# Kernel tuning notes

Measured on AMD Instinct MI355X. Metric: run time of the kernel, lower is better.

The kernel has to match this reference:

```python
import jax, jax.numpy as jnp
import numpy as np

N = 8192        # nodes
IN_DIM = 512
OUT_DIM = 512
NUM_HEADS = 1   # required for view(-1,3)/view(-1,1,1) consistency in original code
K_NEIGH = 16


def setup_inputs() -> dict:
    key = jax.random.key(0)
    k0, k1, k2, k3, k4 = jax.random.split(key, 5)
    s = 1.0 / np.sqrt(IN_DIM)
    h = jax.random.normal(k0, (N, IN_DIM), dtype=jnp.float32)
    # nn.Linear default init: U(-1/sqrt(fan_in), 1/sqrt(fan_in)), bias=False
    Wq = jax.random.uniform(k1, (OUT_DIM * NUM_HEADS, IN_DIM), jnp.float32, -s, s)
    Wk = jax.random.uniform(k2, (OUT_DIM * NUM_HEADS, IN_DIM), jnp.float32, -s, s)
    Wv = jax.random.uniform(k3, (OUT_DIM * NUM_HEADS, IN_DIM), jnp.float32, -s, s)
    Wg = jax.random.uniform(k4, (3 * NUM_HEADS, IN_DIM), jnp.float32, -s, s)
    return {"h": h, "Wq": Wq, "Wk": Wk, "Wv": Wv, "Wg": Wg}


def _knn_edges(coords, k):
    # dgl.knn_graph semantics: each node receives edges from its k nearest
    # points (self included). src = neighbor, dst = query node.
    sq = jnp.sum(coords * coords, axis=-1)                      # [N]
    neg_d2 = 2.0 * (coords @ coords.T) - sq[:, None] - sq[None, :]  # -||xi-xj||^2, [N,N]
    _, idx = jax.lax.top_k(neg_d2, k)                           # [N,k] nearest per row
    n = coords.shape[0]
    src = idx.reshape(-1)                                       # [N*k]
    dst = jnp.repeat(jnp.arange(n, dtype=idx.dtype), k)         # [N*k]
    return src, dst


def reference(h, Wq, Wk, Wv, Wg):
    n = h.shape[0]
    D = OUT_DIM
    scale = jnp.float32(np.sqrt(D))

    Q_h = (h @ Wq.T).reshape(n, NUM_HEADS, D)
    K_h = (h @ Wk.T).reshape(n, NUM_HEADS, D)
    V_h = (h @ Wv.T).reshape(n, NUM_HEADS, D)
    G_h = (h @ Wg.T).reshape(n, NUM_HEADS, 3)

    coords = G_h.reshape(n, 3)  # num_heads == 1
    src, dst = _knn_edges(coords, K_NEIGH)  # E = n * K_NEIGH edges

    # edge-wise attention score: exp(clip((K_src . Q_dst)/sqrt(D), -5, 5))
    score = jnp.sum(K_h[src] * Q_h[dst], axis=-1, keepdims=True)     # [E,1,1]
    score_e = jnp.exp(jnp.clip(score / scale, -5.0, 5.0))

    # distance decay: exp(clip(-||G_src - G_dst|| / sqrt(D), -5, 5))
    dist = -jnp.sqrt(jnp.sum((G_h[src] - G_h[dst]) ** 2, axis=-1) + 1e-6)  # [E,1]
    distance = jnp.exp(jnp.clip(dist / scale, -5.0, 5.0))

    weight = score_e.reshape(-1, 1, 1) * distance.reshape(-1, 1, 1)  # [E,1,1]
    v1 = weight * V_h[src]                                           # [E,1,D]

    wV = jax.ops.segment_sum(v1, dst, num_segments=n)                # [n,1,D]
    z = jax.ops.segment_sum(score_e, dst, num_segments=n)            # [n,1,1]
    z = jnp.broadcast_to(z.reshape(n, 1, 1), (n, 1, D))

    mask = z > 0
    out = jnp.where(mask, wV / jnp.where(mask, z, 1.0), wV)
    return out
```

## Files before the change

kernel.cpp:

```cpp
#include <hip/hip_runtime.h>
#include <hip/hip_bf16.h>
#include <math.h>

#define N_NODES 8192
#define IN_DIM  512
#define OUT_DIM 512
#define KN      16
#define CAP     128
#define QPB     8

typedef __attribute__((ext_vector_type(8))) short bf16x8;
typedef __attribute__((ext_vector_type(4))) float f32x4;

__device__ __forceinline__ ushort f2bf(float x) {
  __hip_bfloat16 b = __float2bfloat16(x);
  return *reinterpret_cast<ushort*>(&b);
}
__device__ __forceinline__ float bflo(unsigned u) { return __uint_as_float(u << 16); }
__device__ __forceinline__ float bfhi(unsigned u) { return __uint_as_float(u & 0xffff0000u); }

#define GLOAD_LDS16(gp, lp)                                                     \
  __builtin_amdgcn_global_load_lds((const __attribute__((address_space(1))) void*)(gp), \
                                   (__attribute__((address_space(3))) void*)(lp), 16, 0, 0)

__global__ __launch_bounds__(256) void prep_kernel(
    const float* __restrict__ h, const float* __restrict__ Wg,
    ushort* __restrict__ A2,
    double* __restrict__ Gx, double* __restrict__ Gy,
    double* __restrict__ Gz, double* __restrict__ Gsq,
    float4* __restrict__ gpk) {
  const int node = (blockIdx.x * 256 + threadIdx.x) >> 6;
  const int lane = threadIdx.x & 63;
  const int k = lane * 8;
  const float* hr = h + (size_t)node * IN_DIM;

  float4 v0 = *(const float4*)&hr[k];
  float4 v1 = *(const float4*)&hr[k + 4];

  ushort h0 = f2bf(v0.x), h1 = f2bf(v0.y), h2 = f2bf(v0.z), h3 = f2bf(v0.w);
  ushort h4 = f2bf(v1.x), h5 = f2bf(v1.y), h6 = f2bf(v1.z), h7 = f2bf(v1.w);
  ushort4 hiA = make_ushort4(h0, h1, h2, h3);
  ushort4 hiB = make_ushort4(h4, h5, h6, h7);
  ushort4 loA = make_ushort4(f2bf(v0.x - bflo((unsigned)h0)), f2bf(v0.y - bflo((unsigned)h1)),
                             f2bf(v0.z - bflo((unsigned)h2)), f2bf(v0.w - bflo((unsigned)h3)));
  ushort4 loB = make_ushort4(f2bf(v1.x - bflo((unsigned)h4)), f2bf(v1.y - bflo((unsigned)h5)),
                             f2bf(v1.z - bflo((unsigned)h6)), f2bf(v1.w - bflo((unsigned)h7)));
  size_t base = (size_t)node * 1024 + k;
  *(ushort4*)&A2[base]           = hiA;
  *(ushort4*)&A2[base + 4]       = hiB;
  *(ushort4*)&A2[base + 512]     = loA;
  *(ushort4*)&A2[base + 512 + 4] = loB;

  float4 w0a = *(const float4*)&Wg[0 * IN_DIM + k];
  float4 w0b = *(const float4*)&Wg[0 * IN_DIM + k + 4];
  float4 w1a = *(const float4*)&Wg[1 * IN_DIM + k];
  float4 w1b = *(const float4*)&Wg[1 * IN_DIM + k + 4];
  float4 w2a = *(const float4*)&Wg[2 * IN_DIM + k];
  float4 w2b = *(const float4*)&Wg[2 * IN_DIM + k + 4];

  double s0 = 0.0, s1 = 0.0, s2 = 0.0;
  s0 += (double)v0.x * w0a.x; s0 += (double)v0.y * w0a.y;
  s0 += (double)v0.z * w0a.z; s0 += (double)v0.w * w0a.w;
  s0 += (double)v1.x * w0b.x; s0 += (double)v1.y * w0b.y;
  s0 += (double)v1.z * w0b.z; s0 += (double)v1.w * w0b.w;
  s1 += (double)v0.x * w1a.x; s1 += (double)v0.y * w1a.y;
  s1 += (double)v0.z * w1a.z; s1 += (double)v0.w * w1a.w;
  s1 += (double)v1.x * w1b.x; s1 += (double)v1.y * w1b.y;
  s1 += (double)v1.z * w1b.z; s1 += (double)v1.w * w1b.w;
  s2 += (double)v0.x * w2a.x; s2 += (double)v0.y * w2a.y;
  s2 += (double)v0.z * w2a.z; s2 += (double)v0.w * w2a.w;
  s2 += (double)v1.x * w2b.x; s2 += (double)v1.y * w2b.y;
  s2 += (double)v1.z * w2b.z; s2 += (double)v1.w * w2b.w;

  #pragma unroll
  for (int off = 32; off; off >>= 1) {
    s0 += __shfl_down(s0, off);
    s1 += __shfl_down(s1, off);
    s2 += __shfl_down(s2, off);
  }
  if (lane == 0) {
    double sq = s0 * s0 + s1 * s1 + s2 * s2;
    Gx[node] = s0; Gy[node] = s1; Gz[node] = s2; Gsq[node] = sq;
    gpk[node] = make_float4((float)s0, (float)s1, (float)s2, -(float)sq);
  }
}

__global__ __launch_bounds__(256) void split_w(const float* __restrict__ Wq,
                                               const float* __restrict__ Wk,
                                               const float* __restrict__ Wv,
                                               ushort* __restrict__ Bqk,
                                               ushort* __restrict__ Bv) {
  int i = blockIdx.x * 256 + threadIdx.x;
  int n  = i >> 7;
  int kc = (i & 127) << 2;
  if (n < 1024) {
    const float* W = (n < 512) ? Wq : Wk;
    int r = n & 511;
    float4 v = *(const float4*)&W[(size_t)r * 512 + kc];
    *(ushort4*)&Bqk[(size_t)n * 512 + kc] =
        make_ushort4(f2bf(v.x), f2bf(v.y), f2bf(v.z), f2bf(v.w));
  } else {
    int r = n - 1024;
    float4 v = *(const float4*)&Wv[(size_t)r * 512 + kc];
    ushort4 hv = make_ushort4(f2bf(v.x), f2bf(v.y), f2bf(v.z), f2bf(v.w));
    *(ushort4*)&Bv[(size_t)r * 1024 + kc]       = hv;
    *(ushort4*)&Bv[(size_t)r * 1024 + 512 + kc] = hv;
  }
}

#define GEMM_BLOCKS 768
#define SM_BYTES 20544

__global__ __launch_bounds__(256) void gemm_knn(
    const ushort* __restrict__ A2, const ushort* __restrict__ Bqk,
    const ushort* __restrict__ Bv,
    ushort* __restrict__ Q2, ushort* __restrict__ K2, ushort* __restrict__ V2,
    const float4* __restrict__ gpk,
    const double* __restrict__ Gx, const double* __restrict__ Gy,
    const double* __restrict__ Gz, const double* __restrict__ Gsq,
    int* __restrict__ knn) {
  __shared__ unsigned long long smraw[SM_BYTES / 8];
  const int tid = threadIdx.x, w = tid >> 6, lane = tid & 63;

  if (blockIdx.x < GEMM_BLOCKS) {
    const int id = blockIdx.x;
    const int sw = (id & 7) * 96 + (id >> 3);
    const int bm = sw / 12, bn = sw % 12;
    const int wr = w >> 1, wc = w & 1;
    const bool isv = (bn >= 8);
    const int  kmax = isv ? 1024 : 512;
    const int  ldb  = isv ? 1024 : 512;
    const ushort* Bb = isv ? (Bv + (size_t)(bn - 8) * 128 * 1024)
                           : (Bqk + (size_t)bn * 128 * 512);
    ushort* lA = (ushort*)smraw;
    ushort* lB = lA + 128 * 32;

    f32x4 acc[4][4] = {};

    const int   srow = w * 32 + (lane >> 2);
    const int   scol = (lane & 3) * 8;
    const size_t gA0 = (size_t)(bm * 128 + srow) * 1024 + scol;
    const size_t gB0 = (size_t)srow * ldb + scol;

    for (int k0 = 0; k0 < kmax; k0 += 32) {
      GLOAD_LDS16(&A2[gA0 + k0],                  &lA[w * 1024]);
      GLOAD_LDS16(&A2[gA0 + 16 * 1024 + k0],      &lA[w * 1024 + 512]);
      GLOAD_LDS16(&Bb[gB0 + k0],                  &lB[w * 1024]);
      GLOAD_LDS16(&Bb[gB0 + (size_t)16 * ldb + k0], &lB[w * 1024 + 512]);
      __syncthreads();

      const int ar = wr * 64 + (lane & 15);
      const int br = wc * 64 + (lane & 15);
      const int kc = (lane >> 4) * 8;
      bf16x8 af[4], bfr[4];
      #pragma unroll
      for (int f = 0; f < 4; ++f) {
        af[f]  = *(const bf16x8*)&lA[(ar + f * 16) * 32 + kc];
        bfr[f] = *(const bf16x8*)&lB[(br + f * 16) * 32 + kc];
      }
      #pragma unroll
      for (int fm = 0; fm < 4; ++fm)
        #pragma unroll
        for (int fn = 0; fn < 4; ++fn)
          acc[fm][fn] = __builtin_amdgcn_mfma_f32_16x16x32_bf16(af[fm], bfr[fn], acc[fm][fn], 0, 0, 0);
      __syncthreads();
    }

    ushort* Cm = isv ? V2 : (bn < 4 ? Q2 : K2);
    const int col  = (isv ? (bn - 8) : (bn & 3)) * 128 + wc * 64 + (lane & 15);
    const int row0 = bm * 128 + wr * 64 + (lane >> 4) * 4;
    #pragma unroll
    for (int fm = 0; fm < 4; ++fm)
      #pragma unroll
      for (int fn = 0; fn < 4; ++fn)
        #pragma unroll
        for (int r = 0; r < 4; ++r)
          Cm[(size_t)(row0 + fm * 16 + r) * 512 + col + fn * 16] = f2bf(acc[fm][fn][r]);
  } else {
    const int qbase = (blockIdx.x - GEMM_BLOCKS) * QPB;
    float (*s_tmax)[256] = (float(*)[256])smraw;
    int   (*s_cand)[CAP] = (int(*)[CAP])((char*)smraw + 8192);
    double(*s_dval)[CAP] = (double(*)[CAP])((char*)smraw + 12288);
    int*   s_cnt = (int*)((char*)smraw + 20480);
    float* s_T   = (float*)((char*)smraw + 20512);

    float q2x[QPB], q2y[QPB], q2z[QPB], tmax[QPB];
    #pragma unroll
    for (int s = 0; s < QPB; ++s) {
      float4 qv = gpk[qbase + s];
      q2x[s] = 2.f * qv.x; q2y[s] = 2.f * qv.y; q2z[s] = 2.f * qv.z;
      tmax[s] = -1e30f;
    }
    if (tid < QPB) s_cnt[tid] = 0;

    {
      float4 c0 = gpk[tid];
      float4 c1 = gpk[tid + 256];
      for (int i = 0; i < 16; ++i) {
        int nx = ((i + 1) & 15) * 512;
        float4 n0 = gpk[tid + nx];
        float4 n1 = gpk[tid + nx + 256];
        #pragma unroll
        for (int s = 0; s < QPB; ++s) {
          float v0 = fmaf(q2x[s], c0.x, fmaf(q2y[s], c0.y, fmaf(q2z[s], c0.z, c0.w)));
          float v1 = fmaf(q2x[s], c1.x, fmaf(q2y[s], c1.y, fmaf(q2z[s], c1.z, c1.w)));
          tmax[s] = fmaxf(fmaxf(tmax[s], v0), v1);
        }
        c0 = n0; c1 = n1;
      }
    }
    #pragma unroll
    for (int s = 0; s < QPB; ++s) s_tmax[s][tid] = tmax[s];
    __syncthreads();

    #pragma unroll
    for (int qq = 0; qq < 2; ++qq) {
      int q = w * 2 + qq;
      float v = fmaxf(fmaxf(s_tmax[q][lane], s_tmax[q][lane + 64]),
                      fmaxf(s_tmax[q][lane + 128], s_tmax[q][lane + 192]));
      unsigned b = __float_as_uint(v);
      unsigned u = b ^ ((unsigned)((int)b >> 31) | 0x80000000u);
      unsigned thr = 0;
      for (int bit = 31; bit >= 0; --bit) {
        unsigned cand = thr | (1u << bit);
        unsigned long long m = __ballot(u >= cand);
        if (__popcll(m) >= KN) thr = cand;
      }
      unsigned tb = (thr & 0x80000000u) ? (thr ^ 0x80000000u) : ~thr;
      if (lane == 0) s_T[q] = __uint_as_float(tb);
    }
    __syncthreads();

    float Ts[QPB];
    #pragma unroll
    for (int s = 0; s < QPB; ++s) Ts[s] = s_T[s];
    {
      float4 c0 = gpk[tid];
      float4 c1 = gpk[tid + 256];
      for (int i = 0; i < 16; ++i) {
        int nx = ((i + 1) & 15) * 512;
        float4 n0 = gpk[tid + nx];
        float4 n1 = gpk[tid + nx + 256];
        int j0 = tid + i * 512, j1 = j0 + 256;
        #pragma unroll
        for (int s = 0; s < QPB; ++s) {
          float v0 = fmaf(q2x[s], c0.x, fmaf(q2y[s], c0.y, fmaf(q2z[s], c0.z, c0.w)));
          float v1 = fmaf(q2x[s], c1.x, fmaf(q2y[s], c1.y, fmaf(q2z[s], c1.z, c1.w)));
          if (v0 >= Ts[s]) { int p = atomicAdd(&s_cnt[s], 1); if (p < CAP) s_cand[s][p] = j0; }
          if (v1 >= Ts[s]) { int p = atomicAdd(&s_cnt[s], 1); if (p < CAP) s_cand[s][p] = j1; }
        }
        c0 = n0; c1 = n1;
      }
    }
    __syncthreads();

    const int qA = w * 2, qB = qA + 1;
    const int cntA = min(s_cnt[qA], CAP);
    const int cntB = min(s_cnt[qB], CAP);
    int j0a = -1, j1a = -1, j0b = -1, j1b = -1;
    double v0a = 0, v1a = 0, v0b = 0, v1b = 0;
    {
      int gq = qbase + qA;
      double xi = Gx[gq], yi = Gy[gq], zi = Gz[gq], sqi = Gsq[gq];
      if (lane < cntA) {
        j0a = s_cand[qA][lane];
        v0a = 2.0 * (xi * Gx[j0a] + yi * Gy[j0a] + zi * Gz[j0a]) - sqi - Gsq[j0a];
        s_dval[qA][lane] = v0a;
      }
      if (lane + 64 < cntA) {
        j1a = s_cand[qA][lane + 64];
        v1a = 2.0 * (xi * Gx[j1a] + yi * Gy[j1a] + zi * Gz[j1a]) - sqi - Gsq[j1a];
        s_dval[qA][lane + 64] = v1a;
      }
    }
    {
      int gq = qbase + qB;
      double xi = Gx[gq], yi = Gy[gq], zi = Gz[gq], sqi = Gsq[gq];
      if (lane < cntB) {
        j0b = s_cand[qB][lane];
        v0b = 2.0 * (xi * Gx[j0b] + yi * Gy[j0b] + zi * Gz[j0b]) - sqi - Gsq[j0b];
        s_dval[qB][lane] = v0b;
      }
      if (lane + 64 < cntB) {
        j1b = s_cand[qB][lane + 64];
        v1b = 2.0 * (xi * Gx[j1b] + yi * Gy[j1b] + zi * Gz[j1b]) - sqi - Gsq[j1b];
        s_dval[qB][lane + 64] = v1b;
      }
    }
    __syncthreads();
    {
      int r0 = 0, r1 = 0;
      for (int m = 0; m < cntA; ++m) {
        double dv = s_dval[qA][m]; int di = s_cand[qA][m];
        r0 += (dv > v0a) || (dv == v0a && di < j0a);
        r1 += (dv > v1a) || (dv == v1a && di < j1a);
      }
      int gq = qbase + qA;
      if (j0a >= 0 && r0 < KN) knn[gq * KN + r0] = j0a;
      if (j1a >= 0 && r1 < KN) knn[gq * KN + r1] = j1a;
    }
    {
      int r0 = 0, r1 = 0;
      for (int m = 0; m < cntB; ++m) {
        double dv = s_dval[qB][m]; int di = s_cand[qB][m];
        r0 += (dv > v0b) || (dv == v0b && di < j0b);
        r1 += (dv > v1b) || (dv == v1b && di < j1b);
      }
      int gq = qbase + qB;
      if (j0b >= 0 && r0 < KN) knn[gq * KN + r0] = j0b;
      if (j1b >= 0 && r1 < KN) knn[gq * KN + r1] = j1b;
    }
  }
}

__global__ __launch_bounds__(256) void attend_kernel(
    const ushort* __restrict__ Q2, const ushort* __restrict__ K2, const ushort* __restrict__ V2,
    const float4* __restrict__ gpk,
    const int* __restrict__ knn, float* __restrict__ out) {
  const int i    = blockIdx.x;
  const int tid  = threadIdx.x;
  const int wv   = tid >> 6;
  const int lane = tid & 63;

  __shared__ int   s_idx[KN];
  __shared__ float s_w[KN];
  __shared__ float s_se[KN];

  if (tid < KN) s_idx[tid] = knn[i * KN + tid];
  __syncthreads();

  uint4 qa = *(const uint4*)&Q2[(size_t)i * 512 + lane * 8];
  float q0 = bflo(qa.x), q1 = bfhi(qa.x), q2 = bflo(qa.y), q3 = bfhi(qa.y);
  float q4 = bflo(qa.z), q5 = bfhi(qa.z), q6 = bflo(qa.w), q7 = bfhi(qa.w);

  float partial[4];
  #pragma unroll
  for (int s = 0; s < 4; ++s) {
    int src = s_idx[wv * 4 + s];
    uint4 ka = *(const uint4*)&K2[(size_t)src * 512 + lane * 8];
    float acc = q0 * bflo(ka.x);
    acc = fmaf(q1, bfhi(ka.x), acc);
    acc = fmaf(q2, bflo(ka.y), acc);
    acc = fmaf(q3, bfhi(ka.y), acc);
    acc = fmaf(q4, bflo(ka.z), acc);
    acc = fmaf(q5, bfhi(ka.z), acc);
    acc = fmaf(q6, bflo(ka.w), acc);
    acc = fmaf(q7, bfhi(ka.w), acc);
    partial[s] = acc;
  }
  #pragma unroll
  for (int s = 0; s < 4; ++s)
    #pragma unroll
    for (int off = 32; off; off >>= 1) partial[s] += __shfl_down(partial[s], off);

  if (lane == 0) {
    float4 gi = gpk[i];
    #pragma unroll
    for (int s = 0; s < 4; ++s) {
      int e = wv * 4 + s;
      int src = s_idx[e];
      float sc = partial[s] / 22.627417f;
      sc = fminf(fmaxf(sc, -5.f), 5.f);
      float se = expf(sc);
      float4 gs = gpk[src];
      float dx = gi.x - gs.x, dy = gi.y - gs.y, dz = gi.z - gs.z;
      float dd = -sqrtf(fmaf(dx, dx, fmaf(dy, dy, fmaf(dz, dz, 1e-6f))));
      float dc = fminf(fmaxf(dd / 22.627417f, -5.f), 5.f);
      float de = expf(dc);
      s_se[e] = se;
      s_w[e]  = se * de;
    }
  }
  __syncthreads();

  float z = 0.f;
  #pragma unroll
  for (int e = 0; e < KN; ++e) z += s_se[e];

  const int d = tid * 2;
  float a0 = 0.f, a1 = 0.f;
  #pragma unroll
  for (int e = 0; e < KN; ++e) {
    unsigned vv = *(const unsigned*)&V2[(size_t)s_idx[e] * 512 + d];
    a0 = fmaf(s_w[e], bflo(vv), a0);
    a1 = fmaf(s_w[e], bfhi(vv), a1);
  }
  float inv = (z > 0.f) ? (1.f / z) : 1.f;
  float2 o = make_float2(a0 * inv, a1 * inv);
  *(float2*)&out[(size_t)i * 512 + d] = o;
}

extern "C" void kernel_launch(void* const* d_in, const int* in_sizes, int n_in,
                              void* d_out, int out_size, void* d_ws, size_t ws_size,
                              hipStream_t stream) {
  const float* h  = (const float*)d_in[0];
  const float* Wq = (const float*)d_in[1];
  const float* Wk = (const float*)d_in[2];
  const float* Wv = (const float*)d_in[3];
  const float* Wg = (const float*)d_in[4];
  float* out = (float*)d_out;

  char* ws = (char*)d_ws;
  ushort* A2  = (ushort*)(ws);
  ushort* Bqk = (ushort*)(ws + (16u << 20));
  ushort* Bv  = (ushort*)(ws + (17u << 20));
  ushort* Q2  = (ushort*)(ws + (18u << 20));
  ushort* K2  = (ushort*)(ws + (26u << 20));
  ushort* V2  = (ushort*)(ws + (34u << 20));
  float4* gpk = (float4*)(ws + (42u << 20));
  double* Gx  = (double*)(ws + (42u << 20) + (1u << 17));
  double* Gy  = Gx + N_NODES;
  double* Gz  = Gy + N_NODES;
  double* Gsq = Gz + N_NODES;
  int*    knn = (int*)(Gsq + N_NODES);

  hipLaunchKernelGGL(prep_kernel, dim3(N_NODES / 4), dim3(256), 0, stream,
                     h, Wg, A2, Gx, Gy, Gz, Gsq, gpk);
  hipLaunchKernelGGL(split_w, dim3(768), dim3(256), 0, stream,
                     Wq, Wk, Wv, Bqk, Bv);
  hipLaunchKernelGGL(gemm_knn, dim3(GEMM_BLOCKS + N_NODES / QPB), dim3(256), 0, stream,
                     A2, Bqk, Bv, Q2, K2, V2, gpk, Gx, Gy, Gz, Gsq, knn);
  hipLaunchKernelGGL(attend_kernel, dim3(N_NODES), dim3(256), 0, stream,
                     Q2, K2, V2, gpk, knn, out);
}
```

Measured before the change: 113.7 us.

## Merge prep and weight-split kernels; separate fused GEMM/KNN into two launches

The h-prep and weight-conversion kernels become one launch with block-index dispatch, which removes one launch and lets the two independent prep jobs run concurrently. The previously fused GEMM+KNN kernel is split into a dedicated QKV GEMM kernel and a separate KNN kernel, each with its own statically sized shared memory. The split gives up the overlap of GEMM and KNN blocks inside one launch and serializes the two phases. In exchange each kernel gets its own resource footprint and occupancy, with no block-index branch.

```diff
diff --git a/kernel.cpp b/kernel.cpp
--- a/kernel.cpp
+++ b/kernel.cpp
@@ -23,293 +23,290 @@
   __builtin_amdgcn_global_load_lds((const __attribute__((address_space(1))) void*)(gp), \
                                    (__attribute__((address_space(3))) void*)(lp), 16, 0, 0)
 
-__global__ __launch_bounds__(256) void prep_kernel(
+__global__ __launch_bounds__(256) void prep_split(
     const float* __restrict__ h, const float* __restrict__ Wg,
-    ushort* __restrict__ A2,
+    const float* __restrict__ Wq, const float* __restrict__ Wk,
+    const float* __restrict__ Wv,
+    ushort* __restrict__ A2, ushort* __restrict__ Bqk, ushort* __restrict__ Bv,
     double* __restrict__ Gx, double* __restrict__ Gy,
     double* __restrict__ Gz, double* __restrict__ Gsq,
     float4* __restrict__ gpk) {
-  const int node = (blockIdx.x * 256 + threadIdx.x) >> 6;
-  const int lane = threadIdx.x & 63;
-  const int k = lane * 8;
-  const float* hr = h + (size_t)node * IN_DIM;
-
-  float4 v0 = *(const float4*)&hr[k];
-  float4 v1 = *(const float4*)&hr[k + 4];
-
-  ushort h0 = f2bf(v0.x), h1 = f2bf(v0.y), h2 = f2bf(v0.z), h3 = f2bf(v0.w);
-  ushort h4 = f2bf(v1.x), h5 = f2bf(v1.y), h6 = f2bf(v1.z), h7 = f2bf(v1.w);
-  ushort4 hiA = make_ushort4(h0, h1, h2, h3);
-  ushort4 hiB = make_ushort4(h4, h5, h6, h7);
-  ushort4 loA = make_ushort4(f2bf(v0.x - bflo((unsigned)h0)), f2bf(v0.y - bflo((unsigned)h1)),
-                             f2bf(v0.z - bflo((unsigned)h2)), f2bf(v0.w - bflo((unsigned)h3)));
-  ushort4 loB = make_ushort4(f2bf(v1.x - bflo((unsigned)h4)), f2bf(v1.y - bflo((unsigned)h5)),
-                             f2bf(v1.z - bflo((unsigned)h6)), f2bf(v1.w - bflo((unsigned)h7)));
-  size_t base = (size_t)node * 1024 + k;
-  *(ushort4*)&A2[base]           = hiA;
-  *(ushort4*)&A2[base + 4]       = hiB;
-  *(ushort4*)&A2[base + 512]     = loA;
-  *(ushort4*)&A2[base + 512 + 4] = loB;
-
-  float4 w0a = *(const float4*)&Wg[0 * IN_DIM + k];
-  float4 w0b = *(const float4*)&Wg[0 * IN_DIM + k + 4];
-  float4 w1a = *(const float4*)&Wg[1 * IN_DIM + k];
-  float4 w1b = *(const float4*)&Wg[1 * IN_DIM + k + 4];
-  float4 w2a = *(const float4*)&Wg[2 * IN_DIM + k];
-  float4 w2b = *(const float4*)&Wg[2 * IN_DIM + k + 4];
-
-  double s0 = 0.0, s1 = 0.0, s2 = 0.0;
-  s0 += (double)v0.x * w0a.x; s0 += (double)v0.y * w0a.y;
-  s0 += (double)v0.z * w0a.z; s0 += (double)v0.w * w0a.w;
-  s0 += (double)v1.x * w0b.x; s0 += (double)v1.y * w0b.y;
-  s0 += (double)v1.z * w0b.z; s0 += (double)v1.w * w0b.w;
-  s1 += (double)v0.x * w1a.x; s1 += (double)v0.y * w1a.y;
-  s1 += (double)v0.z * w1a.z; s1 += (double)v0.w * w1a.w;
-  s1 += (double)v1.x * w1b.x; s1 += (double)v1.y * w1b.y;
-  s1 += (double)v1.z * w1b.z; s1 += (double)v1.w * w1b.w;
-  s2 += (double)v0.x * w2a.x; s2 += (double)v0.y * w2a.y;
-  s2 += (double)v0.z * w2a.z; s2 += (double)v0.w * w2a.w;
-  s2 += (double)v1.x * w2b.x; s2 += (double)v1.y * w2b.y;
-  s2 += (double)v1.z * w2b.z; s2 += (double)v1.w * w2b.w;
-
-  #pragma unroll
-  for (int off = 32; off; off >>= 1) {
-    s0 += __shfl_down(s0, off);
-    s1 += __shfl_down(s1, off);
-    s2 += __shfl_down(s2, off);
-  }
-  if (lane == 0) {
-    double sq = s0 * s0 + s1 * s1 + s2 * s2;
-    Gx[node] = s0; Gy[node] = s1; Gz[node] = s2; Gsq[node] = sq;
-    gpk[node] = make_float4((float)s0, (float)s1, (float)s2, -(float)sq);
-  }
-}
-
-__global__ __launch_bounds__(256) void split_w(const float* __restrict__ Wq,
-                                               const float* __restrict__ Wk,
-                                               const float* __restrict__ Wv,
-                                               ushort* __restrict__ Bqk,
-                                               ushort* __restrict__ Bv) {
-  int i = blockIdx.x * 256 + threadIdx.x;
-  int n  = i >> 7;
-  int kc = (i & 127) << 2;
-  if (n < 1024) {
-    const float* W = (n < 512) ? Wq : Wk;
-    int r = n & 511;
-    float4 v = *(const float4*)&W[(size_t)r * 512 + kc];
-    *(ushort4*)&Bqk[(size_t)n * 512 + kc] =
-        make_ushort4(f2bf(v.x), f2bf(v.y), f2bf(v.z), f2bf(v.w));
+  if (blockIdx.x < 2048) {
+    const int node = (blockIdx.x * 256 + threadIdx.x) >> 6;
+    const int lane = threadIdx.x & 63;
+    const int k = lane * 8;
+    const float* hr = h + (size_t)node * IN_DIM;
+
+    float4 v0 = *(const float4*)&hr[k];
+    float4 v1 = *(const float4*)&hr[k + 4];
+
+    ushort h0 = f2bf(v0.x), h1 = f2bf(v0.y), h2 = f2bf(v0.z), h3 = f2bf(v0.w);
+    ushort h4 = f2bf(v1.x), h5 = f2bf(v1.y), h6 = f2bf(v1.z), h7 = f2bf(v1.w);
+    ushort4 hiA = make_ushort4(h0, h1, h2, h3);
+    ushort4 hiB = make_ushort4(h4, h5, h6, h7);
+    ushort4 loA = make_ushort4(f2bf(v0.x - bflo((unsigned)h0)), f2bf(v0.y - bflo((unsigned)h1)),
+                               f2bf(v0.z - bflo((unsigned)h2)), f2bf(v0.w - bflo((unsigned)h3)));
+    ushort4 loB = make_ushort4(f2bf(v1.x - bflo((unsigned)h4)), f2bf(v1.y - bflo((unsigned)h5)),
+                               f2bf(v1.z - bflo((unsigned)h6)), f2bf(v1.w - bflo((unsigned)h7)));
+    size_t base = (size_t)node * 1024 + k;
+    *(ushort4*)&A2[base]           = hiA;
+    *(ushort4*)&A2[base + 4]       = hiB;
+    *(ushort4*)&A2[base + 512]     = loA;
+    *(ushort4*)&A2[base + 512 + 4] = loB;
+
+    float4 w0a = *(const float4*)&Wg[0 * IN_DIM + k];
+    float4 w0b = *(const float4*)&Wg[0 * IN_DIM + k + 4];
+    float4 w1a = *(const float4*)&Wg[1 * IN_DIM + k];
+    float4 w1b = *(const float4*)&Wg[1 * IN_DIM + k + 4];
+    float4 w2a = *(const float4*)&Wg[2 * IN_DIM + k];
+    float4 w2b = *(const float4*)&Wg[2 * IN_DIM + k + 4];
+
+    double s0 = 0.0, s1 = 0.0, s2 = 0.0;
+    s0 += (double)v0.x * w0a.x; s0 += (double)v0.y * w0a.y;
+    s0 += (double)v0.z * w0a.z; s0 += (double)v0.w * w0a.w;
+    s0 += (double)v1.x * w0b.x; s0 += (double)v1.y * w0b.y;
+    s0 += (double)v1.z * w0b.z; s0 += (double)v1.w * w0b.w;
+    s1 += (double)v0.x * w1a.x; s1 += (double)v0.y * w1a.y;
+    s1 += (double)v0.z * w1a.z; s1 += (double)v0.w * w1a.w;
+    s1 += (double)v1.x * w1b.x; s1 += (double)v1.y * w1b.y;
+    s1 += (double)v1.z * w1b.z; s1 += (double)v1.w * w1b.w;
+    s2 += (double)v0.x * w2a.x; s2 += (double)v0.y * w2a.y;
+    s2 += (double)v0.z * w2a.z; s2 += (double)v0.w * w2a.w;
+    s2 += (double)v1.x * w2b.x; s2 += (double)v1.y * w2b.y;
+    s2 += (double)v1.z * w2b.z; s2 += (double)v1.w * w2b.w;
+
+    #pragma unroll
+    for (int off = 32; off; off >>= 1) {
+      s0 += __shfl_down(s0, off);
+      s1 += __shfl_down(s1, off);
+      s2 += __shfl_down(s2, off);
+    }
+    if (lane == 0) {
+      double sq = s0 * s0 + s1 * s1 + s2 * s2;
+      Gx[node] = s0; Gy[node] = s1; Gz[node] = s2; Gsq[node] = sq;
+      gpk[node] = make_float4((float)s0, (float)s1, (float)s2, -(float)sq);
+    }
   } else {
-    int r = n - 1024;
-    float4 v = *(const float4*)&Wv[(size_t)r * 512 + kc];
-    ushort4 hv = make_ushort4(f2bf(v.x), f2bf(v.y), f2bf(v.z), f2bf(v.w));
-    *(ushort4*)&Bv[(size_t)r * 1024 + kc]       = hv;
-    *(ushort4*)&Bv[(size_t)r * 1024 + 512 + kc] = hv;
-  }
-}
-
-#define GEMM_BLOCKS 768
-#define SM_BYTES 20544
-
-__global__ __launch_bounds__(256) void gemm_knn(
+    int i = (blockIdx.x - 2048) * 256 + threadIdx.x;
+    int n  = i >> 7;
+    int kc = (i & 127) << 2;
+    if (n < 1024) {
+      const float* W = (n < 512) ? Wq : Wk;
+      int r = n & 511;
+      float4 v = *(const float4*)&W[(size_t)r * 512 + kc];
+      *(ushort4*)&Bqk[(size_t)n * 512 + kc] =
+          make_ushort4(f2bf(v.x), f2bf(v.y), f2bf(v.z), f2bf(v.w));
+    } else {
+      int r = n - 1024;
+      float4 v = *(const float4*)&Wv[(size_t)r * 512 + kc];
+      ushort4 hv = make_ushort4(f2bf(v.x), f2bf(v.y), f2bf(v.z), f2bf(v.w));
+      *(ushort4*)&Bv[(size_t)r * 1024 + kc]       = hv;
+      *(ushort4*)&Bv[(size_t)r * 1024 + 512 + kc] = hv;
+    }
+  }
+}
+
+__global__ __launch_bounds__(256) void gemm_qkv(
     const ushort* __restrict__ A2, const ushort* __restrict__ Bqk,
     const ushort* __restrict__ Bv,
-    ushort* __restrict__ Q2, ushort* __restrict__ K2, ushort* __restrict__ V2,
+    ushort* __restrict__ Q2, ushort* __restrict__ K2, ushort* __restrict__ V2) {
+  __shared__ ushort lA[128 * 32];
+  __shared__ ushort lB[128 * 32];
+  const int tid = threadIdx.x, w = tid >> 6, lane = tid & 63;
+  const int id = blockIdx.x;
+  const int sw = (id & 7) * 96 + (id >> 3);
+  const int bm = sw / 12, bn = sw % 12;
+  const int wr = w >> 1, wc = w & 1;
+  const bool isv = (bn >= 8);
+  const int  kmax = isv ? 1024 : 512;
+  const int  ldb  = isv ? 1024 : 512;
+  const ushort* Bb = isv ? (Bv + (size_t)(bn - 8) * 128 * 1024)
+                         : (Bqk + (size_t)bn * 128 * 512);
+
+  f32x4 acc[4][4] = {};
+
+  const int   srow = w * 32 + (lane >> 2);
+  const int   scol = (lane & 3) * 8;
+  const size_t gA0 = (size_t)(bm * 128 + srow) * 1024 + scol;
+  const size_t gB0 = (size_t)srow * ldb + scol;
+
+  for (int k0 = 0; k0 < kmax; k0 += 32) {
+    GLOAD_LDS16(&A2[gA0 + k0],                    &lA[w * 1024]);
+    GLOAD_LDS16(&A2[gA0 + 16 * 1024 + k0],        &lA[w * 1024 + 512]);
+    GLOAD_LDS16(&Bb[gB0 + k0],                    &lB[w * 1024]);
+    GLOAD_LDS16(&Bb[gB0 + (size_t)16 * ldb + k0], &lB[w * 1024 + 512]);
+    __syncthreads();
+
+    const int ar = wr * 64 + (lane & 15);
+    const int br = wc * 64 + (lane & 15);
+    const int kc = (lane >> 4) * 8;
+    bf16x8 af[4], bfr[4];
+    #pragma unroll
+    for (int f = 0; f < 4; ++f) {
+      af[f]  = *(const bf16x8*)&lA[(ar + f * 16) * 32 + kc];
+      bfr[f] = *(const bf16x8*)&lB[(br + f * 16) * 32 + kc];
+    }
+    #pragma unroll
+    for (int fm = 0; fm < 4; ++fm)
+      #pragma unroll
+      for (int fn = 0; fn < 4; ++fn)
+        acc[fm][fn] = __builtin_amdgcn_mfma_f32_16x16x32_bf16(af[fm], bfr[fn], acc[fm][fn], 0, 0, 0);
+    __syncthreads();
+  }
+
+  ushort* Cm = isv ? V2 : (bn < 4 ? Q2 : K2);
+  const int col  = (isv ? (bn - 8) : (bn & 3)) * 128 + wc * 64 + (lane & 15);
+  const int row0 = bm * 128 + wr * 64 + (lane >> 4) * 4;
+  #pragma unroll
+  for (int fm = 0; fm < 4; ++fm)
+    #pragma unroll
+    for (int fn = 0; fn < 4; ++fn)
+      #pragma unroll
+      for (int r = 0; r < 4; ++r)
+        Cm[(size_t)(row0 + fm * 16 + r) * 512 + col + fn * 16] = f2bf(acc[fm][fn][r]);
+}
+
+__global__ __launch_bounds__(256) void knn_kernel(
     const float4* __restrict__ gpk,
     const double* __restrict__ Gx, const double* __restrict__ Gy,
     const double* __restrict__ Gz, const double* __restrict__ Gsq,
     int* __restrict__ knn) {
-  __shared__ unsigned long long smraw[SM_BYTES / 8];
-  const int tid = threadIdx.x, w = tid >> 6, lane = tid & 63;
-
-  if (blockIdx.x < GEMM_BLOCKS) {
-    const int id = blockIdx.x;
-    const int sw = (id & 7) * 96 + (id >> 3);
-    const int bm = sw / 12, bn = sw % 12;
-    const int wr = w >> 1, wc = w & 1;
-    const bool isv = (bn >= 8);
-    const int  kmax = isv ? 1024 : 512;
-    const int  ldb  = isv ? 1024 : 512;
-    const ushort* Bb = isv ? (Bv + (size_t)(bn - 8) * 128 * 1024)
-                           : (Bqk + (size_t)bn * 128 * 512);
-    ushort* lA = (ushort*)smraw;
-    ushort* lB = lA + 128 * 32;
-
-    f32x4 acc[4][4] = {};
-
-    const int   srow = w * 32 + (lane >> 2);
-    const int   scol = (lane & 3) * 8;
-    const size_t gA0 = (size_t)(bm * 128 + srow) * 1024 + scol;
-    const size_t gB0 = (size_t)srow * ldb + scol;
-
-    for (int k0 = 0; k0 < kmax; k0 += 32) {
-      GLOAD_LDS16(&A2[gA0 + k0],                  &lA[w * 1024]);
-      GLOAD_LDS16(&A2[gA0 + 16 * 1024 + k0],      &lA[w * 1024 + 512]);
-      GLOAD_LDS16(&Bb[gB0 + k0],                  &lB[w * 1024]);
-      GLOAD_LDS16(&Bb[gB0 + (size_t)16 * ldb + k0], &lB[w * 1024 + 512]);
-      __syncthreads();
-
-      const int ar = wr * 64 + (lane & 15);
-      const int br = wc * 64 + (lane & 15);
-      const int kc = (lane >> 4) * 8;
-      bf16x8 af[4], bfr[4];
+  const int tid   = threadIdx.x;
+  const int w     = tid >> 6;
+  const int lane  = tid & 63;
+  const int qbase = blockIdx.x * QPB;
+
+  __shared__ float  s_tmax[QPB][256];
+  __shared__ int    s_cand[QPB][CAP];
+  __shared__ double s_dval[QPB][CAP];
+  __shared__ int    s_cnt[QPB];
+  __shared__ float  s_T[QPB];
+
+  float q2x[QPB], q2y[QPB], q2z[QPB], tmax[QPB];
+  #pragma unroll
+  for (int s = 0; s < QPB; ++s) {
+    float4 qv = gpk[qbase + s];
+    q2x[s] = 2.f * qv.x; q2y[s] = 2.f * qv.y; q2z[s] = 2.f * qv.z;
+    tmax[s] = -1e30f;
+  }
+  if (tid < QPB) s_cnt[tid] = 0;
+
+  {
+    float4 c0 = gpk[tid];
+    float4 c1 = gpk[tid + 256];
+    for (int i = 0; i < 16; ++i) {
+      int nx = ((i + 1) & 15) * 512;
+      float4 n0 = gpk[tid + nx];
+      float4 n1 = gpk[tid + nx + 256];
       #pragma unroll
-      for (int f = 0; f < 4; ++f) {
-        af[f]  = *(const bf16x8*)&lA[(ar + f * 16) * 32 + kc];
-        bfr[f] = *(const bf16x8*)&lB[(br + f * 16) * 32 + kc];
+      for (int s = 0; s < QPB; ++s) {
+        float v0 = fmaf(q2x[s], c0.x, fmaf(q2y[s], c0.y, fmaf(q2z[s], c0.z, c0.w)));
+        float v1 = fmaf(q2x[s], c1.x, fmaf(q2y[s], c1.y, fmaf(q2z[s], c1.z, c1.w)));
+        tmax[s] = fmaxf(fmaxf(tmax[s], v0), v1);
       }
+      c0 = n0; c1 = n1;
+    }
+  }
+  #pragma unroll
+  for (int s = 0; s < QPB; ++s) s_tmax[s][tid] = tmax[s];
+  __syncthreads();
+
+  #pragma unroll
+  for (int qq = 0; qq < 2; ++qq) {
+    int q = w * 2 + qq;
+    float v = fmaxf(fmaxf(s_tmax[q][lane], s_tmax[q][lane + 64]),
+                    fmaxf(s_tmax[q][lane + 128], s_tmax[q][lane + 192]));
+    unsigned b = __float_as_uint(v);
+    unsigned u = b ^ ((unsigned)((int)b >> 31) | 0x80000000u);
+    unsigned thr = 0;
+    for (int bit = 31; bit >= 0; --bit) {
+      unsigned cand = thr | (1u << bit);
+      unsigned long long m = __ballot(u >= cand);
+      if (__popcll(m) >= KN) thr = cand;
+    }
+    unsigned tb = (thr & 0x80000000u) ? (thr ^ 0x80000000u) : ~thr;
+    if (lane == 0) s_T[q] = __uint_as_float(tb);
+  }
+  __syncthreads();
+
+  float Ts[QPB];
+  #pragma unroll
+  for (int s = 0; s < QPB; ++s) Ts[s] = s_T[s];
+  {
+    float4 c0 = gpk[tid];
+    float4 c1 = gpk[tid + 256];
+    for (int i = 0; i < 16; ++i) {
+      int nx = ((i + 1) & 15) * 512;
+      float4 n0 = gpk[tid + nx];
+      float4 n1 = gpk[tid + nx + 256];
+      int j0 = tid + i * 512, j1 = j0 + 256;
       #pragma unroll
-      for (int fm = 0; fm < 4; ++fm)
-        #pragma unroll
-        for (int fn = 0; fn < 4; ++fn)
-          acc[fm][fn] = __builtin_amdgcn_mfma_f32_16x16x32_bf16(af[fm], bfr[fn], acc[fm][fn], 0, 0, 0);
-      __syncthreads();
-    }
-
-    ushort* Cm = isv ? V2 : (bn < 4 ? Q2 : K2);
-    const int col  = (isv ? (bn - 8) : (bn & 3)) * 128 + wc * 64 + (lane & 15);
-    const int row0 = bm * 128 + wr * 64 + (lane >> 4) * 4;
-    #pragma unroll
-    for (int fm = 0; fm < 4; ++fm)
-      #pragma unroll
-      for (int fn = 0; fn < 4; ++fn)
-        #pragma unroll
-        for (int r = 0; r < 4; ++r)
-          Cm[(size_t)(row0 + fm * 16 + r) * 512 + col + fn * 16] = f2bf(acc[fm][fn][r]);
-  } else {
-    const int qbase = (blockIdx.x - GEMM_BLOCKS) * QPB;
-    float (*s_tmax)[256] = (float(*)[256])smraw;
-    int   (*s_cand)[CAP] = (int(*)[CAP])((char*)smraw + 8192);
-    double(*s_dval)[CAP] = (double(*)[CAP])((char*)smraw + 12288);
-    int*   s_cnt = (int*)((char*)smraw + 20480);
-    float* s_T   = (float*)((char*)smraw + 20512);
-
-    float q2x[QPB], q2y[QPB], q2z[QPB], tmax[QPB];
-    #pragma unroll
-    for (int s = 0; s < QPB; ++s) {
-      float4 qv = gpk[qbase + s];
-      q2x[s] = 2.f * qv.x; q2y[s] = 2.f * qv.y; q2z[s] = 2.f * qv.z;
-      tmax[s] = -1e30f;
-    }
-    if (tid < QPB) s_cnt[tid] = 0;
-
-    {
-      float4 c0 = gpk[tid];
-      float4 c1 = gpk[tid + 256];
-      for (int i = 0; i < 16; ++i) {
-        int nx = ((i + 1) & 15) * 512;
-        float4 n0 = gpk[tid + nx];
-        float4 n1 = gpk[tid + nx + 256];
-        #pragma unroll
-        for (int s = 0; s < QPB; ++s) {
-          float v0 = fmaf(q2x[s], c0.x, fmaf(q2y[s], c0.y, fmaf(q2z[s], c0.z, c0.w)));
-          float v1 = fmaf(q2x[s], c1.x, fmaf(q2y[s], c1.y, fmaf(q2z[s], c1.z, c1.w)));
-          tmax[s] = fmaxf(fmaxf(tmax[s], v0), v1);
-        }
-        c0 = n0; c1 = n1;
+      for (int s = 0; s < QPB; ++s) {
+        float v0 = fmaf(q2x[s], c0.x, fmaf(q2y[s], c0.y, fmaf(q2z[s], c0.z, c0.w)));
+        float v1 = fmaf(q2x[s], c1.x, fmaf(q2y[s], c1.y, fmaf(q2z[s], c1.z, c1.w)));
+        if (v0 >= Ts[s]) { int p = atomicAdd(&s_cnt[s], 1); if (p < CAP) s_cand[s][p] = j0; }
+        if (v1 >= Ts[s]) { int p = atomicAdd(&s_cnt[s], 1); if (p < CAP) s_cand[s][p] = j1; }
       }
-    }
-    #pragma unroll
-    for (int s = 0; s < QPB; ++s) s_tmax[s][tid] = tmax[s];
-    __syncthreads();
-
-    #pragma unroll
-    for (int qq = 0; qq < 2; ++qq) {
-      int q = w * 2 + qq;
-      float v = fmaxf(fmaxf(s_tmax[q][lane], s_tmax[q][lane + 64]),
-                      fmaxf(s_tmax[q][lane + 128], s_tmax[q][lane + 192]));
-      unsigned b = __float_as_uint(v);
-      unsigned u = b ^ ((unsigned)((int)b >> 31) | 0x80000000u);
-      unsigned thr = 0;
-      for (int bit = 31; bit >= 0; --bit) {
-        unsigned cand = thr | (1u << bit);
-        unsigned long long m = __ballot(u >= cand);
-        if (__popcll(m) >= KN) thr = cand;
-      }
-      unsigned tb = (thr & 0x80000000u) ? (thr ^ 0x80000000u) : ~thr;
-      if (lane == 0) s_T[q] = __uint_as_float(tb);
-    }
-    __syncthreads();
-
-    float Ts[QPB];
-    #pragma unroll
-    for (int s = 0; s < QPB; ++s) Ts[s] = s_T[s];
-    {
-      float4 c0 = gpk[tid];
-      float4 c1 = gpk[tid + 256];
-      for (int i = 0; i < 16; ++i) {
-        int nx = ((i + 1) & 15) * 512;
-        float4 n0 = gpk[tid + nx];
-        float4 n1 = gpk[tid + nx + 256];
-        int j0 = tid + i * 512, j1 = j0 + 256;
-        #pragma unroll
-        for (int s = 0; s < QPB; ++s) {
-          float v0 = fmaf(q2x[s], c0.x, fmaf(q2y[s], c0.y, fmaf(q2z[s], c0.z, c0.w)));
-          float v1 = fmaf(q2x[s], c1.x, fmaf(q2y[s], c1.y, fmaf(q2z[s], c1.z, c1.w)));
-          if (v0 >= Ts[s]) { int p = atomicAdd(&s_cnt[s], 1); if (p < CAP) s_cand[s][p] = j0; }
-          if (v1 >= Ts[s]) { int p = atomicAdd(&s_cnt[s], 1); if (p < CAP) s_cand[s][p] = j1; }
-        }
-        c0 = n0; c1 = n1;
-      }
-    }
-    __syncthreads();
-
-    const int qA = w * 2, qB = qA + 1;
-    const int cntA = min(s_cnt[qA], CAP);
-    const int cntB = min(s_cnt[qB], CAP);
-    int j0a = -1, j1a = -1, j0b = -1, j1b = -1;
-    double v0a = 0, v1a = 0, v0b = 0, v1b = 0;
-    {
-      int gq = qbase + qA;
-      double xi = Gx[gq], yi = Gy[gq], zi = Gz[gq], sqi = Gsq[gq];
-      if (lane < cntA) {
-        j0a = s_cand[qA][lane];
-        v0a = 2.0 * (xi * Gx[j0a] + yi * Gy[j0a] + zi * Gz[j0a]) - sqi - Gsq[j0a];
-        s_dval[qA][lane] = v0a;
-      }
-      if (lane + 64 < cntA) {
-        j1a = s_cand[qA][lane + 64];
-        v1a = 2.0 * (xi * Gx[j1a] + yi * Gy[j1a] + zi * Gz[j1a]) - sqi - Gsq[j1a];
-        s_dval[qA][lane + 64] = v1a;
-      }
-    }
-    {
-      int gq = qbase + qB;
-      double xi = Gx[gq], yi = Gy[gq], zi = Gz[gq], sqi = Gsq[gq];
-      if (lane < cntB) {
-        j0b = s_cand[qB][lane];
-        v0b = 2.0 * (xi * Gx[j0b] + yi * Gy[j0b] + zi * Gz[j0b]) - sqi - Gsq[j0b];
-        s_dval[qB][lane] = v0b;
-      }
-      if (lane + 64 < cntB) {
-        j1b = s_cand[qB][lane + 64];
-        v1b = 2.0 * (xi * Gx[j1b] + yi * Gy[j1b] + zi * Gz[j1b]) - sqi - Gsq[j1b];
-        s_dval[qB][lane + 64] = v1b;
-      }
-    }
-    __syncthreads();
-    {
-      int r0 = 0, r1 = 0;
-      for (int m = 0; m < cntA; ++m) {
-        double dv = s_dval[qA][m]; int di = s_cand[qA][m];
-        r0 += (dv > v0a) || (dv == v0a && di < j0a);
-        r1 += (dv > v1a) || (dv == v1a && di < j1a);
-      }
-      int gq = qbase + qA;
-      if (j0a >= 0 && r0 < KN) knn[gq * KN + r0] = j0a;
-      if (j1a >= 0 && r1 < KN) knn[gq * KN + r1] = j1a;
-    }
-    {
-      int r0 = 0, r1 = 0;
-      for (int m = 0; m < cntB; ++m) {
-        double dv = s_dval[qB][m]; int di = s_cand[qB][m];
-        r0 += (dv > v0b) || (dv == v0b && di < j0b);
-        r1 += (dv > v1b) || (dv == v1b && di < j1b);
-      }
-      int gq = qbase + qB;
-      if (j0b >= 0 && r0 < KN) knn[gq * KN + r0] = j0b;
-      if (j1b >= 0 && r1 < KN) knn[gq * KN + r1] = j1b;
-    }
+      c0 = n0; c1 = n1;
+    }
+  }
+  __syncthreads();
+
+  const int qA = w * 2, qB = qA + 1;
+  const int cntA = min(s_cnt[qA], CAP);
+  const int cntB = min(s_cnt[qB], CAP);
+  int j0a = -1, j1a = -1, j0b = -1, j1b = -1;
+  double v0a = 0, v1a = 0, v0b = 0, v1b = 0;
+  {
+    int gq = qbase + qA;
+    double xi = Gx[gq], yi = Gy[gq], zi = Gz[gq], sqi = Gsq[gq];
+    if (lane < cntA) {
+      j0a = s_cand[qA][lane];
+      v0a = 2.0 * (xi * Gx[j0a] + yi * Gy[j0a] + zi * Gz[j0a]) - sqi - Gsq[j0a];
+      s_dval[qA][lane] = v0a;
+    }
+    if (lane + 64 < cntA) {
+      j1a = s_cand[qA][lane + 64];
+      v1a = 2.0 * (xi * Gx[j1a] + yi * Gy[j1a] + zi * Gz[j1a]) - sqi - Gsq[j1a];
+      s_dval[qA][lane + 64] = v1a;
+    }
+  }
+  {
+    int gq = qbase + qB;
+    double xi = Gx[gq], yi = Gy[gq], zi = Gz[gq], sqi = Gsq[gq];
+    if (lane < cntB) {
+      j0b = s_cand[qB][lane];
+      v0b = 2.0 * (xi * Gx[j0b] + yi * Gy[j0b] + zi * Gz[j0b]) - sqi - Gsq[j0b];
+      s_dval[qB][lane] = v0b;
+    }
+    if (lane + 64 < cntB) {
+      j1b = s_cand[qB][lane + 64];
+      v1b = 2.0 * (xi * Gx[j1b] + yi * Gy[j1b] + zi * Gz[j1b]) - sqi - Gsq[j1b];
+      s_dval[qB][lane + 64] = v1b;
+    }
+  }
+  __syncthreads();
+  {
+    int r0 = 0, r1 = 0;
+    for (int m = 0; m < cntA; ++m) {
+      double dv = s_dval[qA][m]; int di = s_cand[qA][m];
+      r0 += (dv > v0a) || (dv == v0a && di < j0a);
+      r1 += (dv > v1a) || (dv == v1a && di < j1a);
+    }
+    int gq = qbase + qA;
+    if (j0a >= 0 && r0 < KN) knn[gq * KN + r0] = j0a;
+    if (j1a >= 0 && r1 < KN) knn[gq * KN + r1] = j1a;
+  }
+  {
+    int r0 = 0, r1 = 0;
+    for (int m = 0; m < cntB; ++m) {
+      double dv = s_dval[qB][m]; int di = s_cand[qB][m];
+      r0 += (dv > v0b) || (dv == v0b && di < j0b);
+      r1 += (dv > v1b) || (dv == v1b && di < j1b);
+    }
+    int gq = qbase + qB;
+    if (j0b >= 0 && r0 < KN) knn[gq * KN + r0] = j0b;
+    if (j1b >= 0 && r1 < KN) knn[gq * KN + r1] = j1b;
   }
 }
 
@@ -414,12 +411,12 @@
   double* Gsq = Gz + N_NODES;
   int*    knn = (int*)(Gsq + N_NODES);
 
-  hipLaunchKernelGGL(prep_kernel, dim3(N_NODES / 4), dim3(256), 0, stream,
-                     h, Wg, A2, Gx, Gy, Gz, Gsq, gpk);
-  hipLaunchKernelGGL(split_w, dim3(768), dim3(256), 0, stream,
-                     Wq, Wk, Wv, Bqk, Bv);
-  hipLaunchKernelGGL(gemm_knn, dim3(GEMM_BLOCKS + N_NODES / QPB), dim3(256), 0, stream,
-                     A2, Bqk, Bv, Q2, K2, V2, gpk, Gx, Gy, Gz, Gsq, knn);
+  hipLaunchKernelGGL(prep_split, dim3(2048 + 768), dim3(256), 0, stream,
+                     h, Wg, Wq, Wk, Wv, A2, Bqk, Bv, Gx, Gy, Gz, Gsq, gpk);
+  hipLaunchKernelGGL(gemm_qkv, dim3(768), dim3(256), 0, stream,
+                     A2, Bqk, Bv, Q2, K2, V2);
+  hipLaunchKernelGGL(knn_kernel, dim3(N_NODES / QPB), dim3(256), 0, stream,
+                     gpk, Gx, Gy, Gz, Gsq, knn);
   hipLaunchKernelGGL(attend_kernel, dim3(N_NODES), dim3(256), 0, stream,
                      Q2, K2, V2, gpk, knn, out);
 }
```

New measurement: 103.6 us. 1.1x faster.
